# Kernel optimization log

Hardware: AMD Instinct MI355X
Metric: run time of the kernel (lower is better)

Reference implementation:

```python
import jax, jax.numpy as jnp
import numpy as np

T = 0.04
PIC_NUM = 4  # images per identity (hardcoded in SP_loss)


def setup_inputs() -> dict:
    key = jax.random.key(0)
    N, D = 8192, 256  # 2048 identities x 4 images, 256-dim ReID features
    x = jax.random.normal(key, (N, D), dtype=jnp.float32)
    x = x / jnp.linalg.norm(x, axis=1, keepdims=True)  # L2-normalize (cosine sims)
    return {"x": x}


def reference(x):
    N = x.shape[0]
    G = N // PIC_NUM  # number of identity groups
    s = (x @ x.T) / T  # [N, N] scaled similarity matrix

    # Diagonal 4x4 blocks: within-class similarities. [G, 4, 4]
    d4 = s.reshape(G, PIC_NUM, G, PIC_NUM)
    gidx = jnp.arange(G)
    pos = d4[gidx, :, gidx, :]  # [G, 4, 4]

    # hard positive: -T * log( sum_{i,j in class} exp(-dot_ij / T) )  (soft-min)
    hard_pos = -T * jax.nn.logsumexp(-pos.reshape(G, PIC_NUM * PIC_NUM), axis=1)

    # least-hard positive: T * log( sum_i 1 / (sum_j exp(-dot_ij / T)) )
    lse_row = jax.nn.logsumexp(-pos, axis=2)           # [G, 4] = log sum_j exp(-dot/T)
    least_pos = T * jax.nn.logsumexp(-lse_row, axis=1)  # [G]

    # negatives: T * log( sum_{i in class, j not in class} exp(dot_ij / T) )
    col_group = jnp.arange(N) // PIC_NUM              # [N]
    same = col_group[None, :] == gidx[:, None]        # [G, N] same-class column mask
    s3 = s.reshape(G, PIC_NUM, N)
    neg_masked = jnp.where(same[:, None, :], -jnp.inf, s3)
    neg = T * jax.nn.logsumexp(neg_masked.reshape(G, PIC_NUM * N), axis=1)  # [G]

    # Original detaches all three S vectors before forming the loss.
    hard_pos = jax.lax.stop_gradient(hard_pos)
    least_pos = jax.lax.stop_gradient(least_pos)
    neg = jax.lax.stop_gradient(neg)

    # alpha: harmonic mean of (hard, least-hard) when hard >= 0, else 0
    alpha = jnp.where(hard_pos >= 0.0,
                      2.0 * least_pos * hard_pos / (hard_pos + least_pos),
                      0.0)
    margin = alpha * hard_pos + (1.0 - alpha) * least_pos
    # log(1 + exp(z)) == softplus(z), numerically stable, same math
    loss = jnp.mean(jax.nn.softplus((neg - margin) / T))
    return loss
```

## Files before the change

### kernel.cpp

```cpp
#include <hip/hip_runtime.h>
#include <math.h>


#define NROWS 8192
#define DDIM  256
#define NGRP  2048
#define NTB   128
#define NTILES (NTB * (NTB + 1) / 2)
#define T_CONST 0.04f
#define INV_T   25.0f
#define EXP2_SCALE 36.06737602222409f
#define SCALE_QTR 0x7B7B7B7Bu

typedef __attribute__((ext_vector_type(8))) int   i32x8_t;
typedef __attribute__((ext_vector_type(4))) int   i32x4_t;
typedef __attribute__((ext_vector_type(4))) float f32x4_t;

__global__ __launch_bounds__(256) void prep_kernel(const float* __restrict__ x,
                                                   unsigned int* __restrict__ xq,
                                                   float* __restrict__ grpsum,
                                                   float* __restrict__ margin) {
    const int b = blockIdx.x;
    if (b < 2048) {
        int gid = b * 256 + threadIdx.x;
        float4 v = *(const float4*)(x + gid * 4);
        int pk = __builtin_amdgcn_cvt_pk_fp8_f32(v.x * 16.f, v.y * 16.f, 0, false);
        pk = __builtin_amdgcn_cvt_pk_fp8_f32(v.z * 16.f, v.w * 16.f, pk, true);
        xq[gid] = (unsigned int)pk;
        if (gid < NGRP) grpsum[gid] = 0.f;
        return;
    }
    const int g = (b - 2048) * 4 + (threadIdx.x >> 6);
    const int lane = threadIdx.x & 63;
    const float* xr = x + (size_t)g * 4 * DDIM;
    float a[16];
#pragma unroll
    for (int k = 0; k < 16; ++k) a[k] = 0.f;
    for (int e = lane; e < DDIM; e += 64) {
        float vv[4];
        vv[0] = xr[e];
        vv[1] = xr[DDIM + e];
        vv[2] = xr[2 * DDIM + e];
        vv[3] = xr[3 * DDIM + e];
#pragma unroll
        for (int i = 0; i < 4; ++i)
#pragma unroll
            for (int j = 0; j < 4; ++j)
                a[i * 4 + j] = fmaf(vv[i], vv[j], a[i * 4 + j]);
    }
#pragma unroll
    for (int k = 0; k < 16; ++k) {
        float t = a[k];
        t += __shfl_xor(t, 32, 64);
        t += __shfl_xor(t, 16, 64);
        t += __shfl_xor(t, 8, 64);
        t += __shfl_xor(t, 4, 64);
        t += __shfl_xor(t, 2, 64);
        t += __shfl_xor(t, 1, 64);
        a[k] = t;
    }
    if (lane == 0) {
        float pos[16];
#pragma unroll
        for (int k = 0; k < 16; ++k) pos[k] = a[k] * INV_T;

        float mx = -pos[0];
#pragma unroll
        for (int k = 1; k < 16; ++k) mx = fmaxf(mx, -pos[k]);
        float se = 0.f;
#pragma unroll
        for (int k = 0; k < 16; ++k) se += __expf(-pos[k] - mx);
        float hard_pos = -T_CONST * (mx + __logf(se));

        float lse_row[4];
#pragma unroll
        for (int i = 0; i < 4; ++i) {
            float m2 = -pos[i * 4];
#pragma unroll
            for (int j = 1; j < 4; ++j) m2 = fmaxf(m2, -pos[i * 4 + j]);
            float s2 = 0.f;
#pragma unroll
            for (int j = 0; j < 4; ++j) s2 += __expf(-pos[i * 4 + j] - m2);
            lse_row[i] = m2 + __logf(s2);
        }
        float m3 = -lse_row[0];
#pragma unroll
        for (int i = 1; i < 4; ++i) m3 = fmaxf(m3, -lse_row[i]);
        float s3 = 0.f;
#pragma unroll
        for (int i = 0; i < 4; ++i) s3 += __expf(-lse_row[i] - m3);
        float least_pos = T_CONST * (m3 + __logf(s3));

        float alpha = (hard_pos >= 0.f)
                          ? (2.f * least_pos * hard_pos) / (hard_pos + least_pos)
                          : 0.f;
        margin[g] = alpha * hard_pos + (1.f - alpha) * least_pos;
    }
}

__global__ __launch_bounds__(64, 3) void gemm_exp_grpsum(const unsigned char* __restrict__ xq,
                                                         float* __restrict__ grpsum) {
    const int idx = blockIdx.x;
    int ti = (int)((257.0f - sqrtf(66049.0f - 8.0f * (float)idx)) * 0.5f);
    while (ti * (257 - ti) / 2 > idx) --ti;
    while ((ti + 1) * (256 - ti) / 2 <= idx) ++ti;
    const int tj = ti + (idx - ti * (257 - ti) / 2);
    const int row0 = ti * 64;
    const int col0 = tj * 64;
    const bool diag = (ti == tj);

    const int lane = threadIdx.x;
    const int quad = lane >> 4;
    const int l16 = lane & 15;

    f32x4_t acc[4][4];
#pragma unroll
    for (int i = 0; i < 4; ++i)
#pragma unroll
        for (int j = 0; j < 4; ++j)
            acc[i][j] = (f32x4_t){0.f, 0.f, 0.f, 0.f};

#pragma unroll
    for (int ks = 0; ks < 2; ++ks) {
        i32x8_t aF[4], bF[4];
#pragma unroll
        for (int mi = 0; mi < 4; ++mi) {
            const unsigned char* pa =
                xq + ((size_t)(row0 + mi * 16 + l16) << 8) + ks * 128 + quad * 32;
            i32x4_t lo = *(const i32x4_t*)pa;
            i32x4_t hi = *(const i32x4_t*)(pa + 16);
            aF[mi] = __builtin_shufflevector(lo, hi, 0, 1, 2, 3, 4, 5, 6, 7);
        }
#pragma unroll
        for (int ni = 0; ni < 4; ++ni) {
            const unsigned char* pb =
                xq + ((size_t)(col0 + ni * 16 + l16) << 8) + ks * 128 + quad * 32;
            i32x4_t lo = *(const i32x4_t*)pb;
            i32x4_t hi = *(const i32x4_t*)(pb + 16);
            bF[ni] = __builtin_shufflevector(lo, hi, 0, 1, 2, 3, 4, 5, 6, 7);
        }
#pragma unroll
        for (int mi = 0; mi < 4; ++mi)
#pragma unroll
            for (int ni = 0; ni < 4; ++ni)
                acc[mi][ni] = __builtin_amdgcn_mfma_scale_f32_16x16x128_f8f6f4(
                    aF[mi], bF[ni], acc[mi][ni],
                    0, 0,
                    0, (int)SCALE_QTR,
                    0, (int)SCALE_QTR);
    }

    const int rg0 = row0 >> 2;
    const int cg0 = col0 >> 2;
    float rowg[4] = {0.f, 0.f, 0.f, 0.f};
    float colp[4] = {0.f, 0.f, 0.f, 0.f};

    if (!diag) {
#pragma unroll
        for (int mi = 0; mi < 4; ++mi)
#pragma unroll
            for (int reg = 0; reg < 4; ++reg)
#pragma unroll
                for (int ni = 0; ni < 4; ++ni) {
                    float e = exp2f(acc[mi][ni][reg] * EXP2_SCALE);
                    rowg[mi] += e;
                    colp[ni] += e;
                }
    } else {
#pragma unroll
        for (int mi = 0; mi < 4; ++mi) {
            const int rgrp = mi * 4 + quad;
#pragma unroll
            for (int reg = 0; reg < 4; ++reg)
#pragma unroll
                for (int ni = 0; ni < 4; ++ni) {
                    const int cgrp = ni * 4 + (l16 >> 2);
                    float e = (cgrp == rgrp) ? 0.f
                                             : exp2f(acc[mi][ni][reg] * EXP2_SCALE);
                    rowg[mi] += e;
                }
        }
    }

#pragma unroll
    for (int mi = 0; mi < 4; ++mi) {
        float v = rowg[mi];
        v += __shfl_xor(v, 1, 64);
        v += __shfl_xor(v, 2, 64);
        v += __shfl_xor(v, 4, 64);
        v += __shfl_xor(v, 8, 64);
        if (l16 == 0) atomicAdd(&grpsum[rg0 + mi * 4 + quad], v);
    }
    if (!diag) {
#pragma unroll
        for (int ni = 0; ni < 4; ++ni) {
            float v = colp[ni];
            v += __shfl_xor(v, 16, 64);
            v += __shfl_xor(v, 32, 64);
            v += __shfl_xor(v, 1, 64);
            v += __shfl_xor(v, 2, 64);
            if (quad == 0 && (l16 & 3) == 0)
                atomicAdd(&grpsum[cg0 + ni * 4 + (l16 >> 2)], v);
        }
    }
}

__global__ __launch_bounds__(256) void finalize_kernel(const float* __restrict__ grpsum,
                                                       const float* __restrict__ margin,
                                                       float* __restrict__ out) {
    const int tid = threadIdx.x;
    float local = 0.f;
    for (int g = tid; g < NGRP; g += 256) {
        float z = __logf(grpsum[g]) - margin[g] * INV_T;
        float sp = (z > 30.f) ? z : log1pf(__expf(z));
        local += sp;
    }
    local += __shfl_xor(local, 1, 64);
    local += __shfl_xor(local, 2, 64);
    local += __shfl_xor(local, 4, 64);
    local += __shfl_xor(local, 8, 64);
    local += __shfl_xor(local, 16, 64);
    local += __shfl_xor(local, 32, 64);
    __shared__ float wsum[4];
    if ((tid & 63) == 0) wsum[tid >> 6] = local;
    __syncthreads();
    if (tid == 0) out[0] = (wsum[0] + wsum[1] + wsum[2] + wsum[3]) * (1.f / (float)NGRP);
}

extern "C" void kernel_launch(void* const* d_in, const int* in_sizes, int n_in,
                              void* d_out, int out_size, void* d_ws, size_t ws_size,
                              hipStream_t stream) {
    const float* x = (const float*)d_in[0];
    float* out = (float*)d_out;

    unsigned int* xq = (unsigned int*)d_ws;
    float* grpsum = (float*)((char*)d_ws + (size_t)NROWS * DDIM);
    float* margin = grpsum + NGRP;

    prep_kernel<<<2048 + 512, 256, 0, stream>>>(x, xq, grpsum, margin);
    gemm_exp_grpsum<<<NTILES, 64, 0, stream>>>((const unsigned char*)xq, grpsum);
    finalize_kernel<<<1, 256, 0, stream>>>(grpsum, margin, out);
}
```

Baseline: 129.4 us.

## Process four consecutive tiles per workgroup, reusing A fragments across same-row tiles

The GEMM kernel now has each 64-thread workgroup walk four consecutive upper-triangular tiles instead of one. It keeps the A-row fragments in registers and reloads them only when the tile row changes, which cuts global loads and launch count. The prep kernel's quantization blocks also each handle four float4 chunks, shrinking the grid. The tradeoff is a quarter as many workgroups and serialized work inside each one, with launch bounds lowered to 2 waves, so there is less parallelism to hide latency.

```diff
diff --git a/kernel.cpp b/kernel.cpp
--- a/kernel.cpp
+++ b/kernel.cpp
@@ -7,6 +7,8 @@
 #define NGRP  2048
 #define NTB   128
 #define NTILES (NTB * (NTB + 1) / 2)
+#define TPW   4
+#define NWG   (NTILES / TPW)
 #define T_CONST 0.04f
 #define INV_T   25.0f
 #define EXP2_SCALE 36.06737602222409f
@@ -21,16 +23,19 @@
                                                    float* __restrict__ grpsum,
                                                    float* __restrict__ margin) {
     const int b = blockIdx.x;
-    if (b < 2048) {
-        int gid = b * 256 + threadIdx.x;
-        float4 v = *(const float4*)(x + gid * 4);
-        int pk = __builtin_amdgcn_cvt_pk_fp8_f32(v.x * 16.f, v.y * 16.f, 0, false);
-        pk = __builtin_amdgcn_cvt_pk_fp8_f32(v.z * 16.f, v.w * 16.f, pk, true);
-        xq[gid] = (unsigned int)pk;
-        if (gid < NGRP) grpsum[gid] = 0.f;
+    if (b < 512) {
+#pragma unroll
+        for (int it = 0; it < 4; ++it) {
+            int gid = it * 131072 + b * 256 + threadIdx.x;
+            float4 v = *(const float4*)(x + (size_t)gid * 4);
+            int pk = __builtin_amdgcn_cvt_pk_fp8_f32(v.x * 16.f, v.y * 16.f, 0, false);
+            pk = __builtin_amdgcn_cvt_pk_fp8_f32(v.z * 16.f, v.w * 16.f, pk, true);
+            xq[gid] = (unsigned int)pk;
+            if (it == 0 && gid < NGRP) grpsum[gid] = 0.f;
+        }
         return;
     }
-    const int g = (b - 2048) * 4 + (threadIdx.x >> 6);
+    const int g = (b - 512) * 4 + (threadIdx.x >> 6);
     const int lane = threadIdx.x & 63;
     const float* xr = x + (size_t)g * 4 * DDIM;
     float a[16];
@@ -98,110 +103,125 @@
     }
 }
 
-__global__ __launch_bounds__(64, 3) void gemm_exp_grpsum(const unsigned char* __restrict__ xq,
+__global__ __launch_bounds__(64, 2) void gemm_exp_grpsum(const unsigned char* __restrict__ xq,
                                                          float* __restrict__ grpsum) {
-    const int idx = blockIdx.x;
-    int ti = (int)((257.0f - sqrtf(66049.0f - 8.0f * (float)idx)) * 0.5f);
-    while (ti * (257 - ti) / 2 > idx) --ti;
-    while ((ti + 1) * (256 - ti) / 2 <= idx) ++ti;
-    const int tj = ti + (idx - ti * (257 - ti) / 2);
-    const int row0 = ti * 64;
-    const int col0 = tj * 64;
-    const bool diag = (ti == tj);
+    const int idx0 = blockIdx.x * TPW;
+    int ti = (int)((257.0f - sqrtf(66049.0f - 8.0f * (float)idx0)) * 0.5f);
+    while (ti * (257 - ti) / 2 > idx0) --ti;
+    while ((ti + 1) * (256 - ti) / 2 <= idx0) ++ti;
+    int tj = ti + (idx0 - ti * (257 - ti) / 2);
 
     const int lane = threadIdx.x;
     const int quad = lane >> 4;
     const int l16 = lane & 15;
 
-    f32x4_t acc[4][4];
-#pragma unroll
-    for (int i = 0; i < 4; ++i)
-#pragma unroll
-        for (int j = 0; j < 4; ++j)
-            acc[i][j] = (f32x4_t){0.f, 0.f, 0.f, 0.f};
-
-#pragma unroll
-    for (int ks = 0; ks < 2; ++ks) {
-        i32x8_t aF[4], bF[4];
+    i32x8_t aF[2][4];
+    int curTi = -1;
+
+    for (int t = 0; t < TPW; ++t) {
+        const int row0 = ti * 64;
+        const int col0 = tj * 64;
+        const bool diag = (ti == tj);
+
+        if (ti != curTi) {
+            curTi = ti;
+#pragma unroll
+            for (int ks = 0; ks < 2; ++ks)
+#pragma unroll
+                for (int mi = 0; mi < 4; ++mi) {
+                    const unsigned char* pa =
+                        xq + ((size_t)(row0 + mi * 16 + l16) << 8) + ks * 128 + quad * 32;
+                    i32x4_t lo = *(const i32x4_t*)pa;
+                    i32x4_t hi = *(const i32x4_t*)(pa + 16);
+                    aF[ks][mi] = __builtin_shufflevector(lo, hi, 0, 1, 2, 3, 4, 5, 6, 7);
+                }
+        }
+
+        f32x4_t acc[4][4];
+#pragma unroll
+        for (int i = 0; i < 4; ++i)
+#pragma unroll
+            for (int j = 0; j < 4; ++j)
+                acc[i][j] = (f32x4_t){0.f, 0.f, 0.f, 0.f};
+
+#pragma unroll
+        for (int ks = 0; ks < 2; ++ks) {
+            i32x8_t bF[4];
+#pragma unroll
+            for (int ni = 0; ni < 4; ++ni) {
+                const unsigned char* pb =
+                    xq + ((size_t)(col0 + ni * 16 + l16) << 8) + ks * 128 + quad * 32;
+                i32x4_t lo = *(const i32x4_t*)pb;
+                i32x4_t hi = *(const i32x4_t*)(pb + 16);
+                bF[ni] = __builtin_shufflevector(lo, hi, 0, 1, 2, 3, 4, 5, 6, 7);
+            }
+#pragma unroll
+            for (int mi = 0; mi < 4; ++mi)
+#pragma unroll
+                for (int ni = 0; ni < 4; ++ni)
+                    acc[mi][ni] = __builtin_amdgcn_mfma_scale_f32_16x16x128_f8f6f4(
+                        aF[ks][mi], bF[ni], acc[mi][ni],
+                        0, 0,
+                        0, (int)SCALE_QTR,
+                        0, (int)SCALE_QTR);
+        }
+
+        const int rg0 = row0 >> 2;
+        const int cg0 = col0 >> 2;
+        float rowg[4] = {0.f, 0.f, 0.f, 0.f};
+        float colp[4] = {0.f, 0.f, 0.f, 0.f};
+
+        if (!diag) {
+#pragma unroll
+            for (int mi = 0; mi < 4; ++mi)
+#pragma unroll
+                for (int reg = 0; reg < 4; ++reg)
+#pragma unroll
+                    for (int ni = 0; ni < 4; ++ni) {
+                        float e = exp2f(acc[mi][ni][reg] * EXP2_SCALE);
+                        rowg[mi] += e;
+                        colp[ni] += e;
+                    }
+        } else {
+#pragma unroll
+            for (int mi = 0; mi < 4; ++mi) {
+                const int rgrp = mi * 4 + quad;
+#pragma unroll
+                for (int reg = 0; reg < 4; ++reg)
+#pragma unroll
+                    for (int ni = 0; ni < 4; ++ni) {
+                        const int cgrp = ni * 4 + (l16 >> 2);
+                        float e = (cgrp == rgrp) ? 0.f
+                                                 : exp2f(acc[mi][ni][reg] * EXP2_SCALE);
+                        rowg[mi] += e;
+                    }
+            }
+        }
+
 #pragma unroll
         for (int mi = 0; mi < 4; ++mi) {
-            const unsigned char* pa =
-                xq + ((size_t)(row0 + mi * 16 + l16) << 8) + ks * 128 + quad * 32;
-            i32x4_t lo = *(const i32x4_t*)pa;
-            i32x4_t hi = *(const i32x4_t*)(pa + 16);
-            aF[mi] = __builtin_shufflevector(lo, hi, 0, 1, 2, 3, 4, 5, 6, 7);
-        }
-#pragma unroll
-        for (int ni = 0; ni < 4; ++ni) {
-            const unsigned char* pb =
-                xq + ((size_t)(col0 + ni * 16 + l16) << 8) + ks * 128 + quad * 32;
-            i32x4_t lo = *(const i32x4_t*)pb;
-            i32x4_t hi = *(const i32x4_t*)(pb + 16);
-            bF[ni] = __builtin_shufflevector(lo, hi, 0, 1, 2, 3, 4, 5, 6, 7);
-        }
-#pragma unroll
-        for (int mi = 0; mi < 4; ++mi)
-#pragma unroll
-            for (int ni = 0; ni < 4; ++ni)
-                acc[mi][ni] = __builtin_amdgcn_mfma_scale_f32_16x16x128_f8f6f4(
-                    aF[mi], bF[ni], acc[mi][ni],
-                    0, 0,
-                    0, (int)SCALE_QTR,
-                    0, (int)SCALE_QTR);
-    }
-
-    const int rg0 = row0 >> 2;
-    const int cg0 = col0 >> 2;
-    float rowg[4] = {0.f, 0.f, 0.f, 0.f};
-    float colp[4] = {0.f, 0.f, 0.f, 0.f};
-
-    if (!diag) {
-#pragma unroll
-        for (int mi = 0; mi < 4; ++mi)
-#pragma unroll
-            for (int reg = 0; reg < 4; ++reg)
-#pragma unroll
-                for (int ni = 0; ni < 4; ++ni) {
-                    float e = exp2f(acc[mi][ni][reg] * EXP2_SCALE);
-                    rowg[mi] += e;
-                    colp[ni] += e;
-                }
-    } else {
-#pragma unroll
-        for (int mi = 0; mi < 4; ++mi) {
-            const int rgrp = mi * 4 + quad;
-#pragma unroll
-            for (int reg = 0; reg < 4; ++reg)
-#pragma unroll
-                for (int ni = 0; ni < 4; ++ni) {
-                    const int cgrp = ni * 4 + (l16 >> 2);
-                    float e = (cgrp == rgrp) ? 0.f
-                                             : exp2f(acc[mi][ni][reg] * EXP2_SCALE);
-                    rowg[mi] += e;
-                }
-        }
-    }
-
-#pragma unroll
-    for (int mi = 0; mi < 4; ++mi) {
-        float v = rowg[mi];
-        v += __shfl_xor(v, 1, 64);
-        v += __shfl_xor(v, 2, 64);
-        v += __shfl_xor(v, 4, 64);
-        v += __shfl_xor(v, 8, 64);
-        if (l16 == 0) atomicAdd(&grpsum[rg0 + mi * 4 + quad], v);
-    }
-    if (!diag) {
-#pragma unroll
-        for (int ni = 0; ni < 4; ++ni) {
-            float v = colp[ni];
-            v += __shfl_xor(v, 16, 64);
-            v += __shfl_xor(v, 32, 64);
+            float v = rowg[mi];
             v += __shfl_xor(v, 1, 64);
             v += __shfl_xor(v, 2, 64);
-            if (quad == 0 && (l16 & 3) == 0)
-                atomicAdd(&grpsum[cg0 + ni * 4 + (l16 >> 2)], v);
-        }
+            v += __shfl_xor(v, 4, 64);
+            v += __shfl_xor(v, 8, 64);
+            if (l16 == 0) atomicAdd(&grpsum[rg0 + mi * 4 + quad], v);
+        }
+        if (!diag) {
+#pragma unroll
+            for (int ni = 0; ni < 4; ++ni) {
+                float v = colp[ni];
+                v += __shfl_xor(v, 16, 64);
+                v += __shfl_xor(v, 32, 64);
+                v += __shfl_xor(v, 1, 64);
+                v += __shfl_xor(v, 2, 64);
+                if (quad == 0 && (l16 & 3) == 0)
+                    atomicAdd(&grpsum[cg0 + ni * 4 + (l16 >> 2)], v);
+            }
+        }
+
+        ++tj;
+        if (tj == NTB) { ++ti; tj = ti; }
     }
 }
 
@@ -237,7 +257,7 @@
     float* grpsum = (float*)((char*)d_ws + (size_t)NROWS * DDIM);
     float* margin = grpsum + NGRP;
 
-    prep_kernel<<<2048 + 512, 256, 0, stream>>>(x, xq, grpsum, margin);
-    gemm_exp_grpsum<<<NTILES, 64, 0, stream>>>((const unsigned char*)xq, grpsum);
+    prep_kernel<<<1024, 256, 0, stream>>>(x, xq, grpsum, margin);
+    gemm_exp_grpsum<<<NWG, 64, 0, stream>>>((const unsigned char*)xq, grpsum);
     finalize_kernel<<<1, 256, 0, stream>>>(grpsum, margin, out);
 }
```

After: 116.6 us. 9.9% less time.
